# Kernel tuning notes

Hardware: AMD Instinct MI355X
Metric: run time of the kernel (lower is better)

The kernel has to match this reference:

```python
import jax, jax.numpy as jnp
import numpy as np

B, T, D = 128, 2048, 256
LAMDA = 0.5


def setup_inputs() -> dict:
    key = jax.random.key(0)
    ks = jax.random.split(key, 8)
    return {
        "sentiment": jax.random.normal(ks[0], (B, D), jnp.float32),
        "aspect": jax.random.normal(ks[1], (B, D), jnp.float32),
        "sentiment_memory": jax.random.normal(ks[2], (B, T, D), jnp.float32),
        "aspect_memory": jax.random.normal(ks[3], (B, T, D), jnp.float32),
        "mask": jnp.ones((B, T), jnp.float32),
        # MultiplicativeAttention params: rand(D,D)*0.2-0.1, bias zeros(1)
        "W_mul": jax.random.uniform(ks[4], (D, D), jnp.float32) * 0.2 - 0.1,
        "b_mul": jnp.zeros((1,), jnp.float32),
        # AdditiveAttention: Linear(2D, 1) -> weight vector [2D], bias [1]
        "w_ss": jax.random.normal(ks[5], (2 * D,), jnp.float32) * 0.02,
        "b_ss": jnp.zeros((1,), jnp.float32),
        "w_sa": jax.random.normal(ks[6], (2 * D,), jnp.float32) * 0.02,
        "b_sa": jnp.zeros((1,), jnp.float32),
    }


def _masked_norm(scores, mask):
    # exp(scores - max) * mask, normalized (matches torch branch exactly)
    s = scores - jnp.max(scores, axis=1, keepdims=True)
    e = jnp.exp(s) * mask
    return e / jnp.sum(e, axis=1, keepdims=True)


def _additive_attn(query, key_mem, w, b, mask):
    # Linear([key; query_repeated]) == key @ w_k + query @ w_q + b
    d = query.shape[-1]
    scores = key_mem @ w[:d] + (query @ w[d:])[:, None] + b[0]  # [B,T]
    return _masked_norm(scores, mask)


def reference(sentiment, aspect, sentiment_memory, aspect_memory, mask,
              W_mul, b_mul, w_ss, b_ss, w_sa, b_sa):
    # Multiplicative attention over aspect_memory (no mask -> plain softmax)
    mids = aspect @ W_mul.T                                        # W @ q, [B,D]
    a_scores = jnp.tanh(jnp.einsum('btd,bd->bt', aspect_memory, mids) + b_mul[0])
    aspect_attn = jax.nn.softmax(a_scores, axis=1)                 # [B,T]
    new_aspect = jnp.einsum('bt,btd->bd', aspect_attn, aspect_memory)  # [B,D]

    ss_attn = _additive_attn(sentiment, sentiment_memory, w_ss, b_ss, mask)
    sa_attn = _additive_attn(new_aspect, sentiment_memory, w_sa, b_sa, mask)
    s_attn = (1.0 - LAMDA) * ss_attn + LAMDA * sa_attn             # [B,T]

    sentiment_out = jnp.einsum('bt,btd->bd', s_attn, sentiment_memory)[:, None, :]  # [B,1,D]
    aspect_out = aspect + new_aspect                                # [B,D]
    return sentiment_out, aspect_out
```

## Files before the change

kernel.cpp:

```cpp
#include <hip/hip_runtime.h>
#include <math.h>

#define BB 128
#define TT 2048
#define DD 256
#define SPLIT 8
#define ROWS_PER_BLOCK (TT / SPLIT)
#define WAVES 4
#define ROWS_PER_WAVE (ROWS_PER_BLOCK / WAVES)

#define WS_MIDS 0
#define WS_P1ACC (WS_MIDS + BB * DD)
#define WS_P1SUM (WS_P1ACC + BB * SPLIT * DD)
#define WS_P2ACC_SS (WS_P1SUM + BB * SPLIT)
#define WS_P2ACC_SA (WS_P2ACC_SS + BB * SPLIT * DD)
#define WS_P2SUM_SS (WS_P2ACC_SA + BB * SPLIT * DD)
#define WS_P2SUM_SA (WS_P2SUM_SS + BB * SPLIT)

__device__ __forceinline__ float wave_reduce_add(float v) {
    #pragma unroll
    for (int off = 32; off > 0; off >>= 1)
        v += __shfl_xor(v, off, 64);
    return v;
}

__device__ __forceinline__ float dot4(const float4& a, const float4& b) {
    return a.x * b.x + a.y * b.y + a.z * b.z + a.w * b.w;
}

__device__ __forceinline__ float tanh_fast(float x) {
    float ax = fabsf(x);
    float t = __expf(-2.0f * ax);
    float th = (1.0f - t) / (1.0f + t);
    return copysignf(th, x);
}

__global__ __launch_bounds__(DD) void mids_kernel(
    const float* __restrict__ aspect, const float* __restrict__ W,
    float* __restrict__ ws)
{
    const int b = blockIdx.x;
    const int i = threadIdx.x;
    __shared__ float a[DD];
    a[i] = aspect[b * DD + i];
    __syncthreads();
    const float4* wrow = (const float4*)(W + (size_t)i * DD);
    float acc = 0.f;
    #pragma unroll 8
    for (int j4 = 0; j4 < DD / 4; ++j4) {
        float4 w4 = wrow[j4];
        acc += a[4 * j4 + 0] * w4.x + a[4 * j4 + 1] * w4.y +
               a[4 * j4 + 2] * w4.z + a[4 * j4 + 3] * w4.w;
    }
    ws[WS_MIDS + b * DD + i] = acc;
}

__global__ __launch_bounds__(256) void pass_kernel(
    const float* __restrict__ smem_g, const float* __restrict__ amem_g,
    const float* __restrict__ mask, const float* __restrict__ w_ss,
    const float* __restrict__ w_sa, const float* __restrict__ b_mul,
    float* __restrict__ ws)
{
    const int s = blockIdx.x;
    const int b = blockIdx.y;
    const int tid = threadIdx.x;
    const int wave = tid >> 6;
    const int lane = tid & 63;
    const int t0 = s * ROWS_PER_BLOCK + wave * ROWS_PER_WAVE;

    __shared__ __align__(16) float lds_acc[2 * WAVES * DD];
    __shared__ float lds_sum[2 * WAVES];

    if (blockIdx.z == 0) {
        const float4 m4 = *(const float4*)(ws + WS_MIDS + b * DD + lane * 4);
        const float bm = b_mul[0];
        const float* base = amem_g + ((size_t)b * TT + t0) * DD + lane * 4;
        float4 acc = make_float4(0.f, 0.f, 0.f, 0.f);
        float lsum = 0.f;
        for (int r = 0; r < ROWS_PER_WAVE; r += 2) {
            float4 v0 = *(const float4*)(base + (size_t)r * DD);
            float4 v1 = *(const float4*)(base + (size_t)(r + 1) * DD);
            float d0 = wave_reduce_add(dot4(v0, m4));
            float d1 = wave_reduce_add(dot4(v1, m4));
            float e0 = __expf(tanh_fast(d0 + bm));
            float e1 = __expf(tanh_fast(d1 + bm));
            lsum += e0 + e1;
            acc.x += e0 * v0.x + e1 * v1.x;
            acc.y += e0 * v0.y + e1 * v1.y;
            acc.z += e0 * v0.z + e1 * v1.z;
            acc.w += e0 * v0.w + e1 * v1.w;
        }
        ((float4*)(lds_acc + wave * DD))[lane] = acc;
        if (lane == 0) lds_sum[wave] = lsum;
        __syncthreads();
        float tot = lds_acc[0 * DD + tid] + lds_acc[1 * DD + tid] +
                    lds_acc[2 * DD + tid] + lds_acc[3 * DD + tid];
        ws[WS_P1ACC + (size_t)(b * SPLIT + s) * DD + tid] = tot;
        if (tid == 0)
            ws[WS_P1SUM + b * SPLIT + s] =
                lds_sum[0] + lds_sum[1] + lds_sum[2] + lds_sum[3];
    } else {
        const float4 wss4 = *(const float4*)(w_ss + lane * 4);
        const float4 wsa4 = *(const float4*)(w_sa + lane * 4);
        const float* base = smem_g + ((size_t)b * TT + t0) * DD + lane * 4;
        const float* mrow = mask + (size_t)b * TT + t0;
        float4 accss = make_float4(0.f, 0.f, 0.f, 0.f);
        float4 accsa = make_float4(0.f, 0.f, 0.f, 0.f);
        float lss = 0.f, lsa = 0.f;
        for (int r = 0; r < ROWS_PER_WAVE; r += 2) {
            float4 v0 = *(const float4*)(base + (size_t)r * DD);
            float4 v1 = *(const float4*)(base + (size_t)(r + 1) * DD);
            float m0 = mrow[r], m1 = mrow[r + 1];
            float dss0 = wave_reduce_add(dot4(v0, wss4));
            float dss1 = wave_reduce_add(dot4(v1, wss4));
            float dsa0 = wave_reduce_add(dot4(v0, wsa4));
            float dsa1 = wave_reduce_add(dot4(v1, wsa4));
            float ess0 = __expf(dss0) * m0, ess1 = __expf(dss1) * m1;
            float esa0 = __expf(dsa0) * m0, esa1 = __expf(dsa1) * m1;
            lss += ess0 + ess1;
            lsa += esa0 + esa1;
            accss.x += ess0 * v0.x + ess1 * v1.x;
            accss.y += ess0 * v0.y + ess1 * v1.y;
            accss.z += ess0 * v0.z + ess1 * v1.z;
            accss.w += ess0 * v0.w + ess1 * v1.w;
            accsa.x += esa0 * v0.x + esa1 * v1.x;
            accsa.y += esa0 * v0.y + esa1 * v1.y;
            accsa.z += esa0 * v0.z + esa1 * v1.z;
            accsa.w += esa0 * v0.w + esa1 * v1.w;
        }
        ((float4*)(lds_acc + wave * DD))[lane] = accss;
        ((float4*)(lds_acc + (WAVES + wave) * DD))[lane] = accsa;
        if (lane == 0) {
            lds_sum[wave] = lss;
            lds_sum[WAVES + wave] = lsa;
        }
        __syncthreads();
        float tot_ss = lds_acc[0 * DD + tid] + lds_acc[1 * DD + tid] +
                       lds_acc[2 * DD + tid] + lds_acc[3 * DD + tid];
        float tot_sa = lds_acc[(WAVES + 0) * DD + tid] + lds_acc[(WAVES + 1) * DD + tid] +
                       lds_acc[(WAVES + 2) * DD + tid] + lds_acc[(WAVES + 3) * DD + tid];
        ws[WS_P2ACC_SS + (size_t)(b * SPLIT + s) * DD + tid] = tot_ss;
        ws[WS_P2ACC_SA + (size_t)(b * SPLIT + s) * DD + tid] = tot_sa;
        if (tid == 0) {
            ws[WS_P2SUM_SS + b * SPLIT + s] =
                lds_sum[0] + lds_sum[1] + lds_sum[2] + lds_sum[3];
            ws[WS_P2SUM_SA + b * SPLIT + s] =
                lds_sum[4] + lds_sum[5] + lds_sum[6] + lds_sum[7];
        }
    }
}

__global__ __launch_bounds__(DD) void combine_kernel(
    const float* __restrict__ aspect, const float* __restrict__ ws,
    float* __restrict__ out)
{
    const int b = blockIdx.x;
    const int d = threadIdx.x;
    if (blockIdx.y == 0) {
        float acc = 0.f, l = 0.f;
        #pragma unroll
        for (int s = 0; s < SPLIT; ++s)
            acc += ws[WS_P1ACC + (size_t)(b * SPLIT + s) * DD + d];
        #pragma unroll
        for (int s = 0; s < SPLIT; ++s)
            l += ws[WS_P1SUM + b * SPLIT + s];
        out[BB * DD + b * DD + d] = aspect[b * DD + d] + acc / l;
    } else {
        float ass = 0.f, asa = 0.f, lss = 0.f, lsa = 0.f;
        #pragma unroll
        for (int s = 0; s < SPLIT; ++s) {
            ass += ws[WS_P2ACC_SS + (size_t)(b * SPLIT + s) * DD + d];
            asa += ws[WS_P2ACC_SA + (size_t)(b * SPLIT + s) * DD + d];
        }
        #pragma unroll
        for (int s = 0; s < SPLIT; ++s) {
            lss += ws[WS_P2SUM_SS + b * SPLIT + s];
            lsa += ws[WS_P2SUM_SA + b * SPLIT + s];
        }
        out[b * DD + d] = 0.5f * (ass / lss) + 0.5f * (asa / lsa);
    }
}

extern "C" void kernel_launch(void* const* d_in, const int* in_sizes, int n_in,
                              void* d_out, int out_size, void* d_ws, size_t ws_size,
                              hipStream_t stream) {
    (void)in_sizes; (void)n_in; (void)out_size; (void)ws_size;
    const float* aspect = (const float*)d_in[1];
    const float* smem   = (const float*)d_in[2];
    const float* amem   = (const float*)d_in[3];
    const float* mask   = (const float*)d_in[4];
    const float* W_mul  = (const float*)d_in[5];
    const float* b_mul  = (const float*)d_in[6];
    const float* w_ss   = (const float*)d_in[7];
    const float* w_sa   = (const float*)d_in[9];
    float* out = (float*)d_out;
    float* ws  = (float*)d_ws;

    mids_kernel<<<BB, DD, 0, stream>>>(aspect, W_mul, ws);
    pass_kernel<<<dim3(SPLIT, BB, 2), 256, 0, stream>>>(
        smem, amem, mask, w_ss, w_sa, b_mul, ws);
    combine_kernel<<<dim3(BB, 2), DD, 0, stream>>>(aspect, ws, out);
}
```

Measured before the change: 546.4 us.

## Process four rows per wave with 16-lane DPP reductions instead of full-wave shuffles

Each wave now splits into four 16-lane groups, and each group handles its own row. Every lane holds 16 contiguous floats loaded as four float4s. The per-row dot product is reduced within 16 lanes using DPP row operations rather than a six-step 64-lane shuffle reduction, and the cross-group merge happens once after the loop. This cuts shuffle latency and instruction count per row, which matters because the loop is latency-bound on serial reductions. In exchange it raises register usage, since there are 8 to 16 float4 accumulators, and each lane now reads 64 contiguous bytes per row.

```diff
diff --git a/kernel.cpp b/kernel.cpp
--- a/kernel.cpp
+++ b/kernel.cpp
@@ -17,13 +17,6 @@
 #define WS_P2SUM_SS (WS_P2ACC_SA + BB * SPLIT * DD)
 #define WS_P2SUM_SA (WS_P2SUM_SS + BB * SPLIT)
 
-__device__ __forceinline__ float wave_reduce_add(float v) {
-    #pragma unroll
-    for (int off = 32; off > 0; off >>= 1)
-        v += __shfl_xor(v, off, 64);
-    return v;
-}
-
 __device__ __forceinline__ float dot4(const float4& a, const float4& b) {
     return a.x * b.x + a.y * b.y + a.z * b.z + a.w * b.w;
 }
@@ -33,6 +26,33 @@
     float t = __expf(-2.0f * ax);
     float th = (1.0f - t) / (1.0f + t);
     return copysignf(th, x);
+}
+
+__device__ __forceinline__ float red16(float v) {
+    int t;
+    t = __builtin_amdgcn_update_dpp(0, __float_as_int(v), 0xB1, 0xF, 0xF, true);
+    v += __int_as_float(t);
+    t = __builtin_amdgcn_update_dpp(0, __float_as_int(v), 0x4E, 0xF, 0xF, true);
+    v += __int_as_float(t);
+    t = __builtin_amdgcn_update_dpp(0, __float_as_int(v), 0x141, 0xF, 0xF, true);
+    v += __int_as_float(t);
+    t = __builtin_amdgcn_update_dpp(0, __float_as_int(v), 0x140, 0xF, 0xF, true);
+    v += __int_as_float(t);
+    return v;
+}
+
+__device__ __forceinline__ float xmerge(float v) {
+    v += __shfl_xor(v, 16, 64);
+    v += __shfl_xor(v, 32, 64);
+    return v;
+}
+__device__ __forceinline__ void merge4(float4& a) {
+    a.x = xmerge(a.x); a.y = xmerge(a.y);
+    a.z = xmerge(a.z); a.w = xmerge(a.w);
+}
+__device__ __forceinline__ void fma4(float4& a, float s, const float4& v) {
+    a.x = fmaf(s, v.x, a.x); a.y = fmaf(s, v.y, a.y);
+    a.z = fmaf(s, v.z, a.z); a.w = fmaf(s, v.w, a.w);
 }
 
 __global__ __launch_bounds__(DD) void mids_kernel(
@@ -66,31 +86,37 @@
     const int tid = threadIdx.x;
     const int wave = tid >> 6;
     const int lane = tid & 63;
+    const int g = lane >> 4;
+    const int sub = lane & 15;
     const int t0 = s * ROWS_PER_BLOCK + wave * ROWS_PER_WAVE;
 
     __shared__ __align__(16) float lds_acc[2 * WAVES * DD];
     __shared__ float lds_sum[2 * WAVES];
 
     if (blockIdx.z == 0) {
-        const float4 m4 = *(const float4*)(ws + WS_MIDS + b * DD + lane * 4);
+        const float4* mp = (const float4*)(ws + WS_MIDS + b * DD + sub * 16);
+        const float4 m0 = mp[0], m1 = mp[1], m2 = mp[2], m3 = mp[3];
         const float bm = b_mul[0];
-        const float* base = amem_g + ((size_t)b * TT + t0) * DD + lane * 4;
-        float4 acc = make_float4(0.f, 0.f, 0.f, 0.f);
+        const float* base = amem_g + ((size_t)b * TT + t0 + g) * DD + sub * 16;
+        float4 a0 = make_float4(0.f,0.f,0.f,0.f), a1 = a0, a2 = a0, a3 = a0;
         float lsum = 0.f;
-        for (int r = 0; r < ROWS_PER_WAVE; r += 2) {
-            float4 v0 = *(const float4*)(base + (size_t)r * DD);
-            float4 v1 = *(const float4*)(base + (size_t)(r + 1) * DD);
-            float d0 = wave_reduce_add(dot4(v0, m4));
-            float d1 = wave_reduce_add(dot4(v1, m4));
-            float e0 = __expf(tanh_fast(d0 + bm));
-            float e1 = __expf(tanh_fast(d1 + bm));
-            lsum += e0 + e1;
-            acc.x += e0 * v0.x + e1 * v1.x;
-            acc.y += e0 * v0.y + e1 * v1.y;
-            acc.z += e0 * v0.z + e1 * v1.z;
-            acc.w += e0 * v0.w + e1 * v1.w;
-        }
-        ((float4*)(lds_acc + wave * DD))[lane] = acc;
+        for (int r = 0; r < ROWS_PER_WAVE; r += 4) {
+            const float4* p = (const float4*)(base + (size_t)r * DD);
+            float4 v0 = p[0], v1 = p[1], v2 = p[2], v3 = p[3];
+            float pd = (dot4(v0, m0) + dot4(v1, m1)) +
+                       (dot4(v2, m2) + dot4(v3, m3));
+            float d = red16(pd);
+            float e = __expf(tanh_fast(d + bm));
+            lsum += e;
+            fma4(a0, e, v0); fma4(a1, e, v1);
+            fma4(a2, e, v2); fma4(a3, e, v3);
+        }
+        lsum = xmerge(lsum);
+        merge4(a0); merge4(a1); merge4(a2); merge4(a3);
+        if (g == 0) {
+            float4* dst = (float4*)(lds_acc + wave * DD + sub * 16);
+            dst[0] = a0; dst[1] = a1; dst[2] = a2; dst[3] = a3;
+        }
         if (lane == 0) lds_sum[wave] = lsum;
         __syncthreads();
         float tot = lds_acc[0 * DD + tid] + lds_acc[1 * DD + tid] +
@@ -100,36 +126,44 @@
             ws[WS_P1SUM + b * SPLIT + s] =
                 lds_sum[0] + lds_sum[1] + lds_sum[2] + lds_sum[3];
     } else {
-        const float4 wss4 = *(const float4*)(w_ss + lane * 4);
-        const float4 wsa4 = *(const float4*)(w_sa + lane * 4);
-        const float* base = smem_g + ((size_t)b * TT + t0) * DD + lane * 4;
-        const float* mrow = mask + (size_t)b * TT + t0;
-        float4 accss = make_float4(0.f, 0.f, 0.f, 0.f);
-        float4 accsa = make_float4(0.f, 0.f, 0.f, 0.f);
+        const float4* wsp = (const float4*)(w_ss + sub * 16);
+        const float4* wap = (const float4*)(w_sa + sub * 16);
+        const float4 ws0 = wsp[0], ws1 = wsp[1], ws2 = wsp[2], ws3 = wsp[3];
+        const float4 wa0 = wap[0], wa1 = wap[1], wa2 = wap[2], wa3 = wap[3];
+        const float* base = smem_g + ((size_t)b * TT + t0 + g) * DD + sub * 16;
+        const float* mrow = mask + (size_t)b * TT + t0 + g;
+        float4 s0 = make_float4(0.f,0.f,0.f,0.f), s1 = s0, s2 = s0, s3 = s0;
+        float4 q0 = s0, q1 = s0, q2 = s0, q3 = s0;
         float lss = 0.f, lsa = 0.f;
-        for (int r = 0; r < ROWS_PER_WAVE; r += 2) {
-            float4 v0 = *(const float4*)(base + (size_t)r * DD);
-            float4 v1 = *(const float4*)(base + (size_t)(r + 1) * DD);
-            float m0 = mrow[r], m1 = mrow[r + 1];
-            float dss0 = wave_reduce_add(dot4(v0, wss4));
-            float dss1 = wave_reduce_add(dot4(v1, wss4));
-            float dsa0 = wave_reduce_add(dot4(v0, wsa4));
-            float dsa1 = wave_reduce_add(dot4(v1, wsa4));
-            float ess0 = __expf(dss0) * m0, ess1 = __expf(dss1) * m1;
-            float esa0 = __expf(dsa0) * m0, esa1 = __expf(dsa1) * m1;
-            lss += ess0 + ess1;
-            lsa += esa0 + esa1;
-            accss.x += ess0 * v0.x + ess1 * v1.x;
-            accss.y += ess0 * v0.y + ess1 * v1.y;
-            accss.z += ess0 * v0.z + ess1 * v1.z;
-            accss.w += ess0 * v0.w + ess1 * v1.w;
-            accsa.x += esa0 * v0.x + esa1 * v1.x;
-            accsa.y += esa0 * v0.y + esa1 * v1.y;
-            accsa.z += esa0 * v0.z + esa1 * v1.z;
-            accsa.w += esa0 * v0.w + esa1 * v1.w;
-        }
-        ((float4*)(lds_acc + wave * DD))[lane] = accss;
-        ((float4*)(lds_acc + (WAVES + wave) * DD))[lane] = accsa;
+        for (int r = 0; r < ROWS_PER_WAVE; r += 4) {
+            const float4* p = (const float4*)(base + (size_t)r * DD);
+            float4 v0 = p[0], v1 = p[1], v2 = p[2], v3 = p[3];
+            float m = mrow[r];
+            float pds = (dot4(v0, ws0) + dot4(v1, ws1)) +
+                        (dot4(v2, ws2) + dot4(v3, ws3));
+            float pda = (dot4(v0, wa0) + dot4(v1, wa1)) +
+                        (dot4(v2, wa2) + dot4(v3, wa3));
+            float dss = red16(pds);
+            float dsa = red16(pda);
+            float ess = __expf(dss) * m;
+            float esa = __expf(dsa) * m;
+            lss += ess;
+            lsa += esa;
+            fma4(s0, ess, v0); fma4(s1, ess, v1);
+            fma4(s2, ess, v2); fma4(s3, ess, v3);
+            fma4(q0, esa, v0); fma4(q1, esa, v1);
+            fma4(q2, esa, v2); fma4(q3, esa, v3);
+        }
+        lss = xmerge(lss);
+        lsa = xmerge(lsa);
+        merge4(s0); merge4(s1); merge4(s2); merge4(s3);
+        merge4(q0); merge4(q1); merge4(q2); merge4(q3);
+        if (g == 0) {
+            float4* d1 = (float4*)(lds_acc + wave * DD + sub * 16);
+            d1[0] = s0; d1[1] = s1; d1[2] = s2; d1[3] = s3;
+            float4* d2 = (float4*)(lds_acc + (WAVES + wave) * DD + sub * 16);
+            d2[0] = q0; d2[1] = q1; d2[2] = q2; d2[3] = q3;
+        }
         if (lane == 0) {
             lds_sum[wave] = lss;
             lds_sum[WAVES + wave] = lsa;
```

New measurement: 537.5 us. No clear change (-1.6%).
